# Optimization experiments

Hardware: AMD Instinct MI355X
Metric: run time of the kernel (lower is better)

## Reference

```python
import jax, jax.numpy as jnp
import numpy as np

B, N, M = 4, 2048, 2048
D_IN = 1024
H, HS = 16, 64
D_OUT = 1024


def _xavier(key, shape):
    # xavier_uniform over last two dims (fan_in=shape[-2], fan_out=shape[-1])
    fan_in, fan_out = shape[-2], shape[-1]
    limit = float(np.sqrt(6.0 / (fan_in + fan_out)))
    return jax.random.uniform(key, shape, jnp.float32, -limit, limit)


def setup_inputs() -> dict:
    key = jax.random.key(0)
    ks = jax.random.split(key, 7)
    return {
        "query": jax.random.normal(ks[0], (B, N, D_IN), jnp.float32),
        "key": jax.random.normal(ks[1], (B, M, D_IN), jnp.float32),
        "value": jax.random.normal(ks[2], (B, M, D_IN), jnp.float32),
        "query_kernel": _xavier(ks[3], (H, D_IN, HS)),
        "key_kernel": _xavier(ks[4], (H, D_IN, HS)),
        "value_kernel": _xavier(ks[5], (H, D_IN, HS)),
        "projection_kernel": _xavier(ks[6], (H, HS, D_OUT)),
        "projection_bias": jnp.zeros((D_OUT,), jnp.float32),
    }


def reference(query, key, value, query_kernel, key_kernel, value_kernel,
              projection_kernel, projection_bias):
    # per-head projections: (B, N, H, HS)
    q = jnp.einsum('bni,hio->bnho', query, query_kernel)
    k = jnp.einsum('bmi,hio->bmho', key, key_kernel)
    v = jnp.einsum('bmi,hio->bmho', value, value_kernel)
    q = q / jnp.sqrt(jnp.asarray(HS, q.dtype))
    logits = jnp.einsum('bnho,bmho->bhnm', q, k)          # (B, H, N, M)
    attn = jax.nn.softmax(logits, axis=-1)
    mh = jnp.einsum('bhnm,bmhi->bnhi', attn, v)           # (B, N, H, HS)
    out = jnp.einsum('bnhi,hio->bno', mh, projection_kernel) + projection_bias
    return out
```

## Files before the change

kernel.cpp:

```cpp
#include <hip/hip_runtime.h>

typedef __attribute__((ext_vector_type(8))) __bf16 bf16x8;
typedef __attribute__((ext_vector_type(4))) float f32x4;
typedef __attribute__((ext_vector_type(16))) float f32x16;
typedef __attribute__((ext_vector_type(8))) unsigned short u16x8;

__device__ __forceinline__ unsigned short f2bf(float f) {
  unsigned int u = __builtin_bit_cast(unsigned int, f);
  u += 0x7FFFu + ((u >> 16) & 1u);
  return (unsigned short)(u >> 16);
}
__device__ __forceinline__ unsigned int cvtpk(float a, float b) {
  unsigned int r;
  asm("v_cvt_pk_bf16_f32 %0, %1, %2" : "=v"(r) : "v"(a), "v"(b));
  return r;
}

#define KDIM 1024

__global__ __launch_bounds__(256) void prep_all(const float* __restrict__ wq,
                                                const float* __restrict__ wk,
                                                const float* __restrict__ wv,
                                                const float* __restrict__ wp,
                                                unsigned short* __restrict__ Wq,
                                                unsigned short* __restrict__ Wk,
                                                unsigned short* __restrict__ Wv,
                                                unsigned short* __restrict__ Wp,
                                                const float* __restrict__ q,
                                                const float* __restrict__ k,
                                                const float* __restrict__ v,
                                                unsigned short* __restrict__ qb,
                                                unsigned short* __restrict__ kb,
                                                unsigned short* __restrict__ vb) {
  __shared__ float T[64][68];
  const int t = threadIdx.x;
  if (blockIdx.x >= 1024) {
    const int blk = blockIdx.x - 1024;
    const int s3 = blk >> 12;
    const int inner = blk & 4095;
    const float* in = s3 == 0 ? q : (s3 == 1 ? k : v);
    unsigned short* out = s3 == 0 ? qb : (s3 == 1 ? kb : vb);
    const long i = ((long)inner * 256 + t) * 8;
    float4 a = *reinterpret_cast<const float4*>(in + i);
    float4 b = *reinterpret_cast<const float4*>(in + i + 4);
    uint4 o;
    o.x = cvtpk(a.x, a.y);
    o.y = cvtpk(a.z, a.w);
    o.z = cvtpk(b.x, b.y);
    o.w = cvtpk(b.z, b.w);
    *reinterpret_cast<uint4*>(out + i) = o;
    return;
  }
  const int sel = blockIdx.x >> 8;
  const int blk = blockIdx.x & 255;
  const int r = t >> 2, c0 = (t & 3) * 16;
  if (sel < 3) {
    const float* w = sel == 0 ? wq : (sel == 1 ? wk : wv);
    unsigned short* out = sel == 0 ? Wq : (sel == 1 ? Wk : Wv);
    const float scale = sel == 0 ? 0.125f * 1.44269504089f : 1.0f;
    const int h = blk >> 4;
    const int k0 = (blk & 15) * 64;
    const float* src = w + h * 65536 + (k0 + r) * 64 + c0;
#pragma unroll
    for (int e = 0; e < 16; e += 4)
      *reinterpret_cast<float4*>(&T[r][c0 + e]) = *reinterpret_cast<const float4*>(src + e);
    __syncthreads();
    unsigned int pk[8];
#pragma unroll
    for (int e = 0; e < 8; ++e)
      pk[e] = cvtpk(T[c0 + 2 * e][r] * scale, T[c0 + 2 * e + 1][r] * scale);
    unsigned short* dst = out + (h * 64 + r) * 1024 + k0 + c0;
    *reinterpret_cast<uint4*>(dst) = *reinterpret_cast<uint4*>(pk);
    *reinterpret_cast<uint4*>(dst + 8) = *reinterpret_cast<uint4*>(pk + 4);
  } else {
    const int i0 = (blk >> 4) * 64;
    const int o0 = (blk & 15) * 64;
    const float* src = wp + (long)(i0 + r) * 1024 + o0 + c0;
#pragma unroll
    for (int e = 0; e < 16; e += 4)
      *reinterpret_cast<float4*>(&T[r][c0 + e]) = *reinterpret_cast<const float4*>(src + e);
    __syncthreads();
    unsigned int pk[8];
#pragma unroll
    for (int e = 0; e < 8; ++e)
      pk[e] = cvtpk(T[c0 + 2 * e][r], T[c0 + 2 * e + 1][r]);
    unsigned short* dst = Wp + (long)(o0 + r) * 1024 + i0 + c0;
    *reinterpret_cast<uint4*>(dst) = *reinterpret_cast<uint4*>(pk);
    *reinterpret_cast<uint4*>(dst + 8) = *reinterpret_cast<uint4*>(pk + 4);
  }
}

#define STAGE_B(buf, kk)                                                                   \
  _Pragma("unroll") for (int i = 0; i < 4; ++i) {                                          \
    const int seg = w * 4 + i;                                                             \
    const int row = seg * 8 + rowl;                                                        \
    const unsigned short* src =                                                            \
        Wt + (long)(bx * 128 + row) * KDIM + (kk) + ((chnk ^ (row & 7)) * 8);              \
    __builtin_amdgcn_global_load_lds((const __attribute__((address_space(1))) void*)src,   \
                                     (__attribute__((address_space(3))) void*)&Bs[(buf) * 8192 + seg * 512], \
                                     16, 0, 0);                                            \
  }
#define STAGE_A(buf, kk)                                                                   \
  _Pragma("unroll") for (int i = 0; i < 4; ++i) {                                          \
    const int seg = w * 4 + i;                                                             \
    const int row = seg * 8 + rowl;                                                        \
    const unsigned short* src =                                                            \
        Ap + ((long)by * 128 + row) * KDIM + (kk) + ((chnk ^ (row & 7)) * 8);              \
    __builtin_amdgcn_global_load_lds((const __attribute__((address_space(1))) void*)src,   \
                                     (__attribute__((address_space(3))) void*)&As[(buf) * 8192 + seg * 512], \
                                     16, 0, 0);                                            \
  }
#define GEMM_COMPUTE(buf)                                                                  \
  _Pragma("unroll") for (int kc = 0; kc < 2; ++kc) {                                       \
    const int chs = ((kc * 4 + lh) ^ (l15 & 7)) * 8;                                       \
    bf16x8 af[4], bfr[4];                                                                  \
    _Pragma("unroll") for (int mi = 0; mi < 4; ++mi)                                       \
        af[mi] = *reinterpret_cast<const bf16x8*>(&As[(buf) * 8192 + (wr + mi * 16 + l15) * 64 + chs]); \
    _Pragma("unroll") for (int ni = 0; ni < 4; ++ni)                                       \
        bfr[ni] = *reinterpret_cast<const bf16x8*>(&Bs[(buf) * 8192 + (wc + ni * 16 + l15) * 64 + chs]); \
    _Pragma("unroll") for (int mi = 0; mi < 4; ++mi)                                       \
      _Pragma("unroll") for (int ni = 0; ni < 4; ++ni)                                     \
          acc[mi][ni] = __builtin_amdgcn_mfma_f32_16x16x32_bf16(af[mi], bfr[ni], acc[mi][ni], 0, 0, 0); \
  }

__global__ __launch_bounds__(256) void gemm_qkv(const unsigned short* __restrict__ qa,
                                                const unsigned short* __restrict__ ka,
                                                const unsigned short* __restrict__ va,
                                                const unsigned short* __restrict__ Wq,
                                                const unsigned short* __restrict__ Wk,
                                                const unsigned short* __restrict__ Wv,
                                                unsigned short* __restrict__ qo,
                                                unsigned short* __restrict__ ko,
                                                unsigned short* __restrict__ vo) {
  __shared__ unsigned short As[2 * 128 * 64];
  __shared__ unsigned short Bs[2 * 128 * 64];
  const int f = blockIdx.x;
  const int xcd = f & 7;
  const int bx = (f >> 3) & 7;
  const int by8 = (f >> 6) & 7;
  const int z = f >> 9;
  const int by = by8 * 8 + xcd;
  const unsigned short* Ap = z == 0 ? qa : (z == 1 ? ka : va);
  const unsigned short* Wt = z == 0 ? Wq : (z == 1 ? Wk : Wv);
  unsigned short* Cp = z == 0 ? qo : (z == 1 ? ko : vo);
  const int t = threadIdx.x;
  const int lane = t & 63, w = t >> 6;
  const int wr = (w >> 1) * 64, wc = (w & 1) * 64;
  const int l15 = lane & 15, lh = lane >> 4;
  const int rowl = lane >> 3;
  const int chnk = lane & 7;

  f32x4 acc[4][4];
#pragma unroll
  for (int i = 0; i < 4; ++i)
#pragma unroll
    for (int j = 0; j < 4; ++j) acc[i][j] = {0.f, 0.f, 0.f, 0.f};

  STAGE_B(0, 0)
  STAGE_A(0, 0)
  __syncthreads();
  for (int k0 = 0; k0 < KDIM; k0 += 64) {
    const int cur = (k0 >> 6) & 1;
    if (k0 + 64 < KDIM) {
      STAGE_B(cur ^ 1, k0 + 64)
      STAGE_A(cur ^ 1, k0 + 64)
    }
    GEMM_COMPUTE(cur)
    __syncthreads();
  }

  const long rbase = (long)by * 128 + wr;
  const long cbase = (long)bx * 128 + wc;
#pragma unroll
  for (int ni = 0; ni < 4; ++ni) {
    const long col = cbase + ni * 16 + l15;
#pragma unroll
    for (int mi = 0; mi < 4; ++mi) {
      const long row = rbase + mi * 16 + lh * 4;
      if (z == 2) {
        uint2 val;
        val.x = cvtpk(acc[mi][ni][0], acc[mi][ni][1]);
        val.y = cvtpk(acc[mi][ni][2], acc[mi][ni][3]);
        *reinterpret_cast<uint2*>(
            &Cp[(row >> 11) * 2097152 + col * 2048 + (row & 2047)]) = val;
      } else {
#pragma unroll
        for (int j = 0; j < 4; ++j)
          Cp[(row + j) * KDIM + col] = f2bf(acc[mi][ni][j]);
      }
    }
  }
}

__global__ __launch_bounds__(256) void gemm_out(const unsigned short* __restrict__ Ap,
                                                const unsigned short* __restrict__ Wt,
                                                float* __restrict__ Cp,
                                                const float* __restrict__ bias) {
  __shared__ unsigned short As[2 * 128 * 64];
  __shared__ unsigned short Bs[2 * 128 * 64];
  const int f = blockIdx.x;
  const int xcd = f & 7;
  const int bx = (f >> 3) & 7;
  const int by = ((f >> 6) & 7) * 8 + xcd;
  const int t = threadIdx.x;
  const int lane = t & 63, w = t >> 6;
  const int wr = (w >> 1) * 64, wc = (w & 1) * 64;
  const int l15 = lane & 15, lh = lane >> 4;
  const int rowl = lane >> 3;
  const int chnk = lane & 7;

  f32x4 acc[4][4];
#pragma unroll
  for (int i = 0; i < 4; ++i)
#pragma unroll
    for (int j = 0; j < 4; ++j) acc[i][j] = {0.f, 0.f, 0.f, 0.f};

  STAGE_B(0, 0)
  STAGE_A(0, 0)
  __syncthreads();
  for (int k0 = 0; k0 < KDIM; k0 += 64) {
    const int cur = (k0 >> 6) & 1;
    if (k0 + 64 < KDIM) {
      STAGE_B(cur ^ 1, k0 + 64)
      STAGE_A(cur ^ 1, k0 + 64)
    }
    GEMM_COMPUTE(cur)
    __syncthreads();
  }

  const long rbase = (long)by * 128 + wr;
  const long cbase = (long)bx * 128 + wc;
#pragma unroll
  for (int ni = 0; ni < 4; ++ni) {
    const long col = cbase + ni * 16 + l15;
    const float bv = bias[col];
#pragma unroll
    for (int mi = 0; mi < 4; ++mi) {
      const long row = rbase + mi * 16 + lh * 4;
#pragma unroll
      for (int j = 0; j < 4; ++j)
        Cp[(row + j) * KDIM + col] = acc[mi][ni][j] + bv;
    }
  }
}

__global__ __launch_bounds__(256, 2) void attn_k(const unsigned short* __restrict__ Qp,
                                                 const unsigned short* __restrict__ Kp,
                                                 const unsigned short* __restrict__ Vtg,
                                                 unsigned short* __restrict__ Op) {
  constexpr int LST = 72;
  __shared__ unsigned short Kl[64 * LST];
  __shared__ unsigned short Vl[64 * LST];
  const int t = threadIdx.x;
  const int lane = t & 63, w = t >> 6;
  const int l31 = lane & 31;
  const int hi = lane >> 5;
  const int d = blockIdx.x;
  const int xcd = d & 7, ii = d >> 3;
  const int bh = xcd * 8 + (ii >> 3);
  const int qblk = ii & 7;
  const long base = (long)(bh >> 4) * 2097152 + (long)(bh & 15) * 64;
  const long vbase = (long)bh * 131072;
  const int n0 = qblk * 256;
  const int sr = t >> 2, sc = (t & 3) * 16;

  bf16x8 qbA[4], qbB[4];
  {
    const unsigned short* qA = Qp + base + (long)(n0 + w * 64 + l31) * 1024 + hi * 8;
    const unsigned short* qB = qA + 32 * 1024;
#pragma unroll
    for (int kc = 0; kc < 4; ++kc) {
      qbA[kc] = *reinterpret_cast<const bf16x8*>(qA + kc * 16);
      qbB[kc] = *reinterpret_cast<const bf16x8*>(qB + kc * 16);
    }
  }

  const unsigned short* ksrc = Kp + base + (long)sr * 1024 + sc;
  const unsigned short* vsrc = Vtg + vbase + (long)sr * 2048 + sc;
  u16x8 kr0 = *reinterpret_cast<const u16x8*>(ksrc);
  u16x8 kr1 = *reinterpret_cast<const u16x8*>(ksrc + 8);
  u16x8 vr0 = *reinterpret_cast<const u16x8*>(vsrc);
  u16x8 vr1 = *reinterpret_cast<const u16x8*>(vsrc + 8);

  float lsumA = 0.f, lsumB = 0.f;
  f32x16 accA0, accA1, accB0, accB1;
#pragma unroll
  for (int r = 0; r < 16; ++r) { accA0[r] = 0.f; accA1[r] = 0.f; accB0[r] = 0.f; accB1[r] = 0.f; }

  for (int m0 = 0; m0 < 2048; m0 += 64) {
    *reinterpret_cast<u16x8*>(&Kl[sr * LST + sc]) = kr0;
    *reinterpret_cast<u16x8*>(&Kl[sr * LST + sc + 8]) = kr1;
    *reinterpret_cast<u16x8*>(&Vl[sr * LST + sc]) = vr0;
    *reinterpret_cast<u16x8*>(&Vl[sr * LST + sc + 8]) = vr1;
    __syncthreads();
    if (m0 + 64 < 2048) {
      kr0 = *reinterpret_cast<const u16x8*>(ksrc + (long)(m0 + 64) * 1024);
      kr1 = *reinterpret_cast<const u16x8*>(ksrc + (long)(m0 + 64) * 1024 + 8);
      vr0 = *reinterpret_cast<const u16x8*>(vsrc + m0 + 64);
      vr1 = *reinterpret_cast<const u16x8*>(vsrc + m0 + 72);
    }

    f32x16 sA0, sA1, sB0, sB1;
#pragma unroll
    for (int r = 0; r < 16; ++r) { sA0[r] = 0.f; sA1[r] = 0.f; sB0[r] = 0.f; sB1[r] = 0.f; }
    __builtin_amdgcn_s_setprio(1);
#pragma unroll
    for (int kc = 0; kc < 4; ++kc) {
      bf16x8 ka0 = *reinterpret_cast<const bf16x8*>(&Kl[(l31) * LST + kc * 16 + hi * 8]);
      bf16x8 ka1 = *reinterpret_cast<const bf16x8*>(&Kl[(32 + l31) * LST + kc * 16 + hi * 8]);
      sA0 = __builtin_amdgcn_mfma_f32_32x32x16_bf16(ka0, qbA[kc], sA0, 0, 0, 0);
      sA1 = __builtin_amdgcn_mfma_f32_32x32x16_bf16(ka1, qbA[kc], sA1, 0, 0, 0);
      sB0 = __builtin_amdgcn_mfma_f32_32x32x16_bf16(ka0, qbB[kc], sB0, 0, 0, 0);
      sB1 = __builtin_amdgcn_mfma_f32_32x32x16_bf16(ka1, qbB[kc], sB1, 0, 0, 0);
    }
    __builtin_amdgcn_s_setprio(0);

    float lstA = 0.f, lstB = 0.f;
#pragma unroll
    for (int r = 0; r < 16; ++r) {
      sA0[r] = __builtin_amdgcn_exp2f(sA0[r]);
      sA1[r] = __builtin_amdgcn_exp2f(sA1[r]);
      lstA += sA0[r] + sA1[r];
      sB0[r] = __builtin_amdgcn_exp2f(sB0[r]);
      sB1[r] = __builtin_amdgcn_exp2f(sB1[r]);
      lstB += sB0[r] + sB1[r];
    }
    lsumA += lstA;
    lsumB += lstB;

    unsigned int WA0[8], WA1[8], WB0[8], WB1[8];
#pragma unroll
    for (int j = 0; j < 8; ++j) {
      WA0[j] = cvtpk(sA0[2 * j], sA0[2 * j + 1]);
      WA1[j] = cvtpk(sA1[2 * j], sA1[2 * j + 1]);
      WB0[j] = cvtpk(sB0[2 * j], sB0[2 * j + 1]);
      WB1[j] = cvtpk(sB1[2 * j], sB1[2 * j + 1]);
    }

    __builtin_amdgcn_s_setprio(1);
#pragma unroll
    for (int kc4 = 0; kc4 < 4; ++kc4) {
      const unsigned int* WmA = (kc4 < 2) ? WA0 : WA1;
      const unsigned int* WmB = (kc4 < 2) ? WB0 : WB1;
      const int b = 4 * (kc4 & 1);
      unsigned int a1 = (unsigned int)__shfl_xor((int)(hi ? WmA[b] : WmA[b + 2]), 32);
      unsigned int a2 = (unsigned int)__shfl_xor((int)(hi ? WmA[b + 1] : WmA[b + 3]), 32);
      unsigned int b1 = (unsigned int)__shfl_xor((int)(hi ? WmB[b] : WmB[b + 2]), 32);
      unsigned int b2 = (unsigned int)__shfl_xor((int)(hi ? WmB[b + 1] : WmB[b + 3]), 32);
      union { unsigned int u[4]; bf16x8 v; } cA, cB;
      cA.u[0] = hi ? a1 : WmA[b];
      cA.u[1] = hi ? a2 : WmA[b + 1];
      cA.u[2] = hi ? WmA[b + 2] : a1;
      cA.u[3] = hi ? WmA[b + 3] : a2;
      cB.u[0] = hi ? b1 : WmB[b];
      cB.u[1] = hi ? b2 : WmB[b + 1];
      cB.u[2] = hi ? WmB[b + 2] : b1;
      cB.u[3] = hi ? WmB[b + 3] : b2;
      bf16x8 vb0 = *reinterpret_cast<const bf16x8*>(&Vl[(l31) * LST + kc4 * 16 + hi * 8]);
      bf16x8 vb1 = *reinterpret_cast<const bf16x8*>(&Vl[(32 + l31) * LST + kc4 * 16 + hi * 8]);
      accA0 = __builtin_amdgcn_mfma_f32_32x32x16_bf16(cA.v, vb0, accA0, 0, 0, 0);
      accA1 = __builtin_amdgcn_mfma_f32_32x32x16_bf16(cA.v, vb1, accA1, 0, 0, 0);
      accB0 = __builtin_amdgcn_mfma_f32_32x32x16_bf16(cB.v, vb0, accB0, 0, 0, 0);
      accB1 = __builtin_amdgcn_mfma_f32_32x32x16_bf16(cB.v, vb1, accB1, 0, 0, 0);
    }
    __builtin_amdgcn_s_setprio(0);
    __syncthreads();
  }

  lsumA += __shfl_xor(lsumA, 32);
  lsumB += __shfl_xor(lsumB, 32);
  float linvA = 1.f / lsumA;
  float linvB = 1.f / lsumB;
#pragma unroll
  for (int r = 0; r < 16; ++r) {
    const int qrow = (r & 3) + 8 * (r >> 2) + 4 * hi;
    float lrA = __shfl(linvA, qrow);
    float lrB = __shfl(linvB, qrow);
    const long rowA = n0 + w * 64 + qrow;
    const long rowB = rowA + 32;
    Op[base + rowA * 1024 + l31] = f2bf(accA0[r] * lrA);
    Op[base + rowA * 1024 + 32 + l31] = f2bf(accA1[r] * lrA);
    Op[base + rowB * 1024 + l31] = f2bf(accB0[r] * lrB);
    Op[base + rowB * 1024 + 32 + l31] = f2bf(accB1[r] * lrB);
  }
}

extern "C" void kernel_launch(void* const* d_in, const int* in_sizes, int n_in,
                              void* d_out, int out_size, void* d_ws, size_t ws_size,
                              hipStream_t stream) {
  const float* q    = (const float*)d_in[0];
  const float* k    = (const float*)d_in[1];
  const float* v    = (const float*)d_in[2];
  const float* wq   = (const float*)d_in[3];
  const float* wk   = (const float*)d_in[4];
  const float* wv   = (const float*)d_in[5];
  const float* wp   = (const float*)d_in[6];
  const float* bias = (const float*)d_in[7];

  unsigned short* ws = (unsigned short*)d_ws;
  unsigned short* Wq = ws;
  unsigned short* Wk = Wq + (1 << 20);
  unsigned short* Wv = Wk + (1 << 20);
  unsigned short* Wp = Wv + (1 << 20);
  unsigned short* qp = Wp + (1 << 20);
  unsigned short* kp = qp + (8 << 20);
  unsigned short* vt = kp + (8 << 20);
  unsigned short* mh = vt + (8 << 20);

  unsigned short* qb16 = (unsigned short*)d_out;
  unsigned short* kb16 = qb16 + (8 << 20);
  unsigned short* vb16 = mh;

  prep_all<<<13312, 256, 0, stream>>>(wq, wk, wv, wp, Wq, Wk, Wv, Wp,
                                      q, k, v, qb16, kb16, vb16);

  gemm_qkv<<<1536, 256, 0, stream>>>(qb16, kb16, vb16, Wq, Wk, Wv, qp, kp, vt);

  attn_k<<<512, 256, 0, stream>>>(qp, kp, vt, mh);

  gemm_out<<<512, 256, 0, stream>>>(mh, Wp, (float*)d_out, bias);
}
```

Before: 183.1 us.

## Double-buffer K/V tiles in LDS to drop one barrier per iteration

Splits the K and V shared-memory tiles into two buffers. The next tile's registers are stored into the alternate buffer after the QK MFMAs, and the following tile's global loads are issued after the PV MFMAs. This removes one __syncthreads per iteration and overlaps the LDS writes with the softmax work. In exchange it doubles LDS use, and the global prefetch now has less compute to hide behind before it is consumed.

Measured after the change: 183.6 us. No clear change (+0.3%).

```diff
diff --git a/kernel.cpp b/kernel.cpp
--- a/kernel.cpp
+++ b/kernel.cpp
@@ -249,8 +249,8 @@
                                                  const unsigned short* __restrict__ Vtg,
                                                  unsigned short* __restrict__ Op) {
   constexpr int LST = 72;
-  __shared__ unsigned short Kl[64 * LST];
-  __shared__ unsigned short Vl[64 * LST];
+  __shared__ unsigned short Kl[2][64 * LST];
+  __shared__ unsigned short Vl[2][64 * LST];
   const int t = threadIdx.x;
   const int lane = t & 63, w = t >> 6;
   const int l31 = lane & 31;
@@ -277,28 +277,30 @@
 
   const unsigned short* ksrc = Kp + base + (long)sr * 1024 + sc;
   const unsigned short* vsrc = Vtg + vbase + (long)sr * 2048 + sc;
+
   u16x8 kr0 = *reinterpret_cast<const u16x8*>(ksrc);
   u16x8 kr1 = *reinterpret_cast<const u16x8*>(ksrc + 8);
   u16x8 vr0 = *reinterpret_cast<const u16x8*>(vsrc);
   u16x8 vr1 = *reinterpret_cast<const u16x8*>(vsrc + 8);
+  *reinterpret_cast<u16x8*>(&Kl[0][sr * LST + sc]) = kr0;
+  *reinterpret_cast<u16x8*>(&Kl[0][sr * LST + sc + 8]) = kr1;
+  *reinterpret_cast<u16x8*>(&Vl[0][sr * LST + sc]) = vr0;
+  *reinterpret_cast<u16x8*>(&Vl[0][sr * LST + sc + 8]) = vr1;
+  kr0 = *reinterpret_cast<const u16x8*>(ksrc + 64 * 1024);
+  kr1 = *reinterpret_cast<const u16x8*>(ksrc + 64 * 1024 + 8);
+  vr0 = *reinterpret_cast<const u16x8*>(vsrc + 64);
+  vr1 = *reinterpret_cast<const u16x8*>(vsrc + 72);
+  __syncthreads();
 
   float lsumA = 0.f, lsumB = 0.f;
   f32x16 accA0, accA1, accB0, accB1;
 #pragma unroll
   for (int r = 0; r < 16; ++r) { accA0[r] = 0.f; accA1[r] = 0.f; accB0[r] = 0.f; accB1[r] = 0.f; }
 
-  for (int m0 = 0; m0 < 2048; m0 += 64) {
-    *reinterpret_cast<u16x8*>(&Kl[sr * LST + sc]) = kr0;
-    *reinterpret_cast<u16x8*>(&Kl[sr * LST + sc + 8]) = kr1;
-    *reinterpret_cast<u16x8*>(&Vl[sr * LST + sc]) = vr0;
-    *reinterpret_cast<u16x8*>(&Vl[sr * LST + sc + 8]) = vr1;
-    __syncthreads();
-    if (m0 + 64 < 2048) {
-      kr0 = *reinterpret_cast<const u16x8*>(ksrc + (long)(m0 + 64) * 1024);
-      kr1 = *reinterpret_cast<const u16x8*>(ksrc + (long)(m0 + 64) * 1024 + 8);
-      vr0 = *reinterpret_cast<const u16x8*>(vsrc + m0 + 64);
-      vr1 = *reinterpret_cast<const u16x8*>(vsrc + m0 + 72);
-    }
+  for (int tI = 0; tI < 32; ++tI) {
+    const int cur = tI & 1;
+    const unsigned short* Kc = &Kl[cur][0];
+    const unsigned short* Vc = &Vl[cur][0];
 
     f32x16 sA0, sA1, sB0, sB1;
 #pragma unroll
@@ -306,14 +308,23 @@
     __builtin_amdgcn_s_setprio(1);
 #pragma unroll
     for (int kc = 0; kc < 4; ++kc) {
-      bf16x8 ka0 = *reinterpret_cast<const bf16x8*>(&Kl[(l31) * LST + kc * 16 + hi * 8]);
-      bf16x8 ka1 = *reinterpret_cast<const bf16x8*>(&Kl[(32 + l31) * LST + kc * 16 + hi * 8]);
+      bf16x8 ka0 = *reinterpret_cast<const bf16x8*>(&Kc[(l31) * LST + kc * 16 + hi * 8]);
+      bf16x8 ka1 = *reinterpret_cast<const bf16x8*>(&Kc[(32 + l31) * LST + kc * 16 + hi * 8]);
       sA0 = __builtin_amdgcn_mfma_f32_32x32x16_bf16(ka0, qbA[kc], sA0, 0, 0, 0);
       sA1 = __builtin_amdgcn_mfma_f32_32x32x16_bf16(ka1, qbA[kc], sA1, 0, 0, 0);
       sB0 = __builtin_amdgcn_mfma_f32_32x32x16_bf16(ka0, qbB[kc], sB0, 0, 0, 0);
       sB1 = __builtin_amdgcn_mfma_f32_32x32x16_bf16(ka1, qbB[kc], sB1, 0, 0, 0);
     }
     __builtin_amdgcn_s_setprio(0);
+
+    if (tI < 31) {
+      unsigned short* Kn = &Kl[cur ^ 1][0];
+      unsigned short* Vn = &Vl[cur ^ 1][0];
+      *reinterpret_cast<u16x8*>(&Kn[sr * LST + sc]) = kr0;
+      *reinterpret_cast<u16x8*>(&Kn[sr * LST + sc + 8]) = kr1;
+      *reinterpret_cast<u16x8*>(&Vn[sr * LST + sc]) = vr0;
+      *reinterpret_cast<u16x8*>(&Vn[sr * LST + sc + 8]) = vr1;
+    }
 
     float lstA = 0.f, lstB = 0.f;
 #pragma unroll
@@ -356,14 +367,22 @@
       cB.u[1] = hi ? b2 : WmB[b + 1];
       cB.u[2] = hi ? WmB[b + 2] : b1;
       cB.u[3] = hi ? WmB[b + 3] : b2;
-      bf16x8 vb0 = *reinterpret_cast<const bf16x8*>(&Vl[(l31) * LST + kc4 * 16 + hi * 8]);
-      bf16x8 vb1 = *reinterpret_cast<const bf16x8*>(&Vl[(32 + l31) * LST + kc4 * 16 + hi * 8]);
+      bf16x8 vb0 = *reinterpret_cast<const bf16x8*>(&Vc[(l31) * LST + kc4 * 16 + hi * 8]);
+      bf16x8 vb1 = *reinterpret_cast<const bf16x8*>(&Vc[(32 + l31) * LST + kc4 * 16 + hi * 8]);
       accA0 = __builtin_amdgcn_mfma_f32_32x32x16_bf16(cA.v, vb0, accA0, 0, 0, 0);
       accA1 = __builtin_amdgcn_mfma_f32_32x32x16_bf16(cA.v, vb1, accA1, 0, 0, 0);
       accB0 = __builtin_amdgcn_mfma_f32_32x32x16_bf16(cB.v, vb0, accB0, 0, 0, 0);
       accB1 = __builtin_amdgcn_mfma_f32_32x32x16_bf16(cB.v, vb1, accB1, 0, 0, 0);
     }
     __builtin_amdgcn_s_setprio(0);
+
+    if (tI < 30) {
+      const long off = (long)(tI + 2) * 64;
+      kr0 = *reinterpret_cast<const u16x8*>(ksrc + off * 1024);
+      kr1 = *reinterpret_cast<const u16x8*>(ksrc + off * 1024 + 8);
+      vr0 = *reinterpret_cast<const u16x8*>(vsrc + off);
+      vr1 = *reinterpret_cast<const u16x8*>(vsrc + off + 8);
+    }
     __syncthreads();
   }
 
```

## Software-pipeline attention loop: overlap QK of tile t with PV of tile t-1

Applied to the files above, without the earlier changes.

Restructures the attention inner loop into a software pipeline. Each iteration computes QK^T MFMAs for the current tile while running the PV MFMAs for the previous tile's softmaxed probabilities, held in ping-pong P registers. K is double-buffered and V triple-buffered in LDS so there is one barrier per iteration. It also seeds the first QK MFMA with a zero constant instead of zero-initialising the accumulators. The aim is to hide exp/convert latency behind matrix work, at the cost of more registers and LDS, which may reduce occupancy.

Result: slower. 395.6 us (+116.0%).

```diff
diff --git a/kernel.cpp b/kernel.cpp
--- a/kernel.cpp
+++ b/kernel.cpp
@@ -249,8 +249,8 @@
                                                  const unsigned short* __restrict__ Vtg,
                                                  unsigned short* __restrict__ Op) {
   constexpr int LST = 72;
-  __shared__ unsigned short Kl[64 * LST];
-  __shared__ unsigned short Vl[64 * LST];
+  __shared__ unsigned short Kl[2][64 * LST];
+  __shared__ unsigned short Vl[3][64 * LST];
   const int t = threadIdx.x;
   const int lane = t & 63, w = t >> 6;
   const int l31 = lane & 31;
@@ -264,6 +264,10 @@
   const int n0 = qblk * 256;
   const int sr = t >> 2, sc = (t & 3) * 16;
 
+  f32x16 FZERO;
+#pragma unroll
+  for (int r = 0; r < 16; ++r) FZERO[r] = 0.f;
+
   bf16x8 qbA[4], qbB[4];
   {
     const unsigned short* qA = Qp + base + (long)(n0 + w * 64 + l31) * 1024 + hi * 8;
@@ -277,95 +281,144 @@
 
   const unsigned short* ksrc = Kp + base + (long)sr * 1024 + sc;
   const unsigned short* vsrc = Vtg + vbase + (long)sr * 2048 + sc;
+
+  float lsumA = 0.f, lsumB = 0.f;
+  f32x16 accA0 = FZERO, accA1 = FZERO, accB0 = FZERO, accB1 = FZERO;
+  unsigned int P0[32], P1[32];
+
+#define DO_QK(tI)                                                                          \
+  {                                                                                        \
+    const unsigned short* Kc = &Kl[(tI) & 1][0];                                           \
+    __builtin_amdgcn_s_setprio(1);                                                         \
+    {                                                                                      \
+      bf16x8 ka0 = *reinterpret_cast<const bf16x8*>(&Kc[(l31) * LST + hi * 8]);            \
+      bf16x8 ka1 = *reinterpret_cast<const bf16x8*>(&Kc[(32 + l31) * LST + hi * 8]);       \
+      sA0 = __builtin_amdgcn_mfma_f32_32x32x16_bf16(ka0, qbA[0], FZERO, 0, 0, 0);          \
+      sA1 = __builtin_amdgcn_mfma_f32_32x32x16_bf16(ka1, qbA[0], FZERO, 0, 0, 0);          \
+      sB0 = __builtin_amdgcn_mfma_f32_32x32x16_bf16(ka0, qbB[0], FZERO, 0, 0, 0);          \
+      sB1 = __builtin_amdgcn_mfma_f32_32x32x16_bf16(ka1, qbB[0], FZERO, 0, 0, 0);          \
+    }                                                                                      \
+    _Pragma("unroll") for (int kc = 1; kc < 4; ++kc) {                                     \
+      bf16x8 ka0 = *reinterpret_cast<const bf16x8*>(&Kc[(l31) * LST + kc * 16 + hi * 8]);  \
+      bf16x8 ka1 = *reinterpret_cast<const bf16x8*>(&Kc[(32 + l31) * LST + kc * 16 + hi * 8]); \
+      sA0 = __builtin_amdgcn_mfma_f32_32x32x16_bf16(ka0, qbA[kc], sA0, 0, 0, 0);           \
+      sA1 = __builtin_amdgcn_mfma_f32_32x32x16_bf16(ka1, qbA[kc], sA1, 0, 0, 0);           \
+      sB0 = __builtin_amdgcn_mfma_f32_32x32x16_bf16(ka0, qbB[kc], sB0, 0, 0, 0);           \
+      sB1 = __builtin_amdgcn_mfma_f32_32x32x16_bf16(ka1, qbB[kc], sB1, 0, 0, 0);           \
+    }                                                                                      \
+    __builtin_amdgcn_s_setprio(0);                                                         \
+  }
+
+#define DO_STAGE(kb, vb)                                                                   \
+  {                                                                                        \
+    *reinterpret_cast<u16x8*>(&Kl[kb][sr * LST + sc]) = kr0;                               \
+    *reinterpret_cast<u16x8*>(&Kl[kb][sr * LST + sc + 8]) = kr1;                           \
+    *reinterpret_cast<u16x8*>(&Vl[vb][sr * LST + sc]) = vr0;                               \
+    *reinterpret_cast<u16x8*>(&Vl[vb][sr * LST + sc + 8]) = vr1;                           \
+  }
+
+#define DO_PV(PR, vb)                                                                      \
+  {                                                                                        \
+    const unsigned short* Vc = &Vl[vb][0];                                                 \
+    __builtin_amdgcn_s_setprio(1);                                                         \
+    _Pragma("unroll") for (int kc4 = 0; kc4 < 4; ++kc4) {                                  \
+      const int offA = (kc4 < 2) ? 0 : 8;                                                  \
+      const int offB = offA + 16;                                                          \
+      const int b = 4 * (kc4 & 1);                                                         \
+      unsigned int a1 = (unsigned int)__shfl_xor((int)(hi ? PR[offA + b] : PR[offA + b + 2]), 32); \
+      unsigned int a2 = (unsigned int)__shfl_xor((int)(hi ? PR[offA + b + 1] : PR[offA + b + 3]), 32); \
+      unsigned int b1 = (unsigned int)__shfl_xor((int)(hi ? PR[offB + b] : PR[offB + b + 2]), 32); \
+      unsigned int b2 = (unsigned int)__shfl_xor((int)(hi ? PR[offB + b + 1] : PR[offB + b + 3]), 32); \
+      union { unsigned int u[4]; bf16x8 v; } cA, cB;                                       \
+      cA.u[0] = hi ? a1 : PR[offA + b];                                                    \
+      cA.u[1] = hi ? a2 : PR[offA + b + 1];                                                \
+      cA.u[2] = hi ? PR[offA + b + 2] : a1;                                                \
+      cA.u[3] = hi ? PR[offA + b + 3] : a2;                                                \
+      cB.u[0] = hi ? b1 : PR[offB + b];                                                    \
+      cB.u[1] = hi ? b2 : PR[offB + b + 1];                                                \
+      cB.u[2] = hi ? PR[offB + b + 2] : b1;                                                \
+      cB.u[3] = hi ? PR[offB + b + 3] : b2;                                                \
+      bf16x8 vb0 = *reinterpret_cast<const bf16x8*>(&Vc[(l31) * LST + kc4 * 16 + hi * 8]); \
+      bf16x8 vb1 = *reinterpret_cast<const bf16x8*>(&Vc[(32 + l31) * LST + kc4 * 16 + hi * 8]); \
+      accA0 = __builtin_amdgcn_mfma_f32_32x32x16_bf16(cA.v, vb0, accA0, 0, 0, 0);          \
+      accA1 = __builtin_amdgcn_mfma_f32_32x32x16_bf16(cA.v, vb1, accA1, 0, 0, 0);          \
+      accB0 = __builtin_amdgcn_mfma_f32_32x32x16_bf16(cB.v, vb0, accB0, 0, 0, 0);          \
+      accB1 = __builtin_amdgcn_mfma_f32_32x32x16_bf16(cB.v, vb1, accB1, 0, 0, 0);          \
+    }                                                                                      \
+    __builtin_amdgcn_s_setprio(0);                                                         \
+  }
+
+#define DO_SOFTMAX(PW)                                                                     \
+  {                                                                                        \
+    float lstA = 0.f, lstB = 0.f;                                                          \
+    _Pragma("unroll") for (int r = 0; r < 16; ++r) {                                       \
+      sA0[r] = __builtin_amdgcn_exp2f(sA0[r]);                                             \
+      sA1[r] = __builtin_amdgcn_exp2f(sA1[r]);                                             \
+      lstA += sA0[r] + sA1[r];                                                             \
+      sB0[r] = __builtin_amdgcn_exp2f(sB0[r]);                                             \
+      sB1[r] = __builtin_amdgcn_exp2f(sB1[r]);                                             \
+      lstB += sB0[r] + sB1[r];                                                             \
+    }                                                                                      \
+    lsumA += lstA;                                                                         \
+    lsumB += lstB;                                                                         \
+    _Pragma("unroll") for (int j = 0; j < 8; ++j) {                                        \
+      PW[j]      = cvtpk(sA0[2 * j], sA0[2 * j + 1]);                                      \
+      PW[8 + j]  = cvtpk(sA1[2 * j], sA1[2 * j + 1]);                                      \
+      PW[16 + j] = cvtpk(sB0[2 * j], sB0[2 * j + 1]);                                      \
+      PW[24 + j] = cvtpk(sB1[2 * j], sB1[2 * j + 1]);                                      \
+    }                                                                                      \
+  }
+
+#define DO_PREFETCH(nt)                                                                    \
+  {                                                                                        \
+    const long off = (long)(nt) * 64;                                                      \
+    kr0 = *reinterpret_cast<const u16x8*>(ksrc + off * 1024);                              \
+    kr1 = *reinterpret_cast<const u16x8*>(ksrc + off * 1024 + 8);                          \
+    vr0 = *reinterpret_cast<const u16x8*>(vsrc + off);                                     \
+    vr1 = *reinterpret_cast<const u16x8*>(vsrc + off + 8);                                 \
+  }
+
+#define BODY(tI, PW, PR)                                                                   \
+  {                                                                                        \
+    f32x16 sA0, sA1, sB0, sB1;                                                             \
+    DO_QK(tI)                                                                              \
+    if ((tI) < 31) DO_STAGE(((tI) + 1) & 1, ((tI) + 1) % 3)                                \
+    DO_PV(PR, ((tI) + 2) % 3)                                                              \
+    DO_SOFTMAX(PW)                                                                         \
+    if ((tI) < 30) DO_PREFETCH((tI) + 2)                                                   \
+    __syncthreads();                                                                       \
+  }
+
   u16x8 kr0 = *reinterpret_cast<const u16x8*>(ksrc);
   u16x8 kr1 = *reinterpret_cast<const u16x8*>(ksrc + 8);
   u16x8 vr0 = *reinterpret_cast<const u16x8*>(vsrc);
   u16x8 vr1 = *reinterpret_cast<const u16x8*>(vsrc + 8);
-
-  float lsumA = 0.f, lsumB = 0.f;
-  f32x16 accA0, accA1, accB0, accB1;
-#pragma unroll
-  for (int r = 0; r < 16; ++r) { accA0[r] = 0.f; accA1[r] = 0.f; accB0[r] = 0.f; accB1[r] = 0.f; }
-
-  for (int m0 = 0; m0 < 2048; m0 += 64) {
-    *reinterpret_cast<u16x8*>(&Kl[sr * LST + sc]) = kr0;
-    *reinterpret_cast<u16x8*>(&Kl[sr * LST + sc + 8]) = kr1;
-    *reinterpret_cast<u16x8*>(&Vl[sr * LST + sc]) = vr0;
-    *reinterpret_cast<u16x8*>(&Vl[sr * LST + sc + 8]) = vr1;
+  DO_STAGE(0, 0)
+  DO_PREFETCH(1)
+  __syncthreads();
+  {
+    f32x16 sA0, sA1, sB0, sB1;
+    DO_QK(0)
+    DO_STAGE(1, 1)
+    DO_SOFTMAX(P0)
+    DO_PREFETCH(2)
     __syncthreads();
-    if (m0 + 64 < 2048) {
-      kr0 = *reinterpret_cast<const u16x8*>(ksrc + (long)(m0 + 64) * 1024);
-      kr1 = *reinterpret_cast<const u16x8*>(ksrc + (long)(m0 + 64) * 1024 + 8);
-      vr0 = *reinterpret_cast<const u16x8*>(vsrc + m0 + 64);
-      vr1 = *reinterpret_cast<const u16x8*>(vsrc + m0 + 72);
-    }
-
-    f32x16 sA0, sA1, sB0, sB1;
-#pragma unroll
-    for (int r = 0; r < 16; ++r) { sA0[r] = 0.f; sA1[r] = 0.f; sB0[r] = 0.f; sB1[r] = 0.f; }
-    __builtin_amdgcn_s_setprio(1);
-#pragma unroll
-    for (int kc = 0; kc < 4; ++kc) {
-      bf16x8 ka0 = *reinterpret_cast<const bf16x8*>(&Kl[(l31) * LST + kc * 16 + hi * 8]);
-      bf16x8 ka1 = *reinterpret_cast<const bf16x8*>(&Kl[(32 + l31) * LST + kc * 16 + hi * 8]);
-      sA0 = __builtin_amdgcn_mfma_f32_32x32x16_bf16(ka0, qbA[kc], sA0, 0, 0, 0);
-      sA1 = __builtin_amdgcn_mfma_f32_32x32x16_bf16(ka1, qbA[kc], sA1, 0, 0, 0);
-      sB0 = __builtin_amdgcn_mfma_f32_32x32x16_bf16(ka0, qbB[kc], sB0, 0, 0, 0);
-      sB1 = __builtin_amdgcn_mfma_f32_32x32x16_bf16(ka1, qbB[kc], sB1, 0, 0, 0);
-    }
-    __builtin_amdgcn_s_setprio(0);
-
-    float lstA = 0.f, lstB = 0.f;
-#pragma unroll
-    for (int r = 0; r < 16; ++r) {
-      sA0[r] = __builtin_amdgcn_exp2f(sA0[r]);
-      sA1[r] = __builtin_amdgcn_exp2f(sA1[r]);
-      lstA += sA0[r] + sA1[r];
-      sB0[r] = __builtin_amdgcn_exp2f(sB0[r]);
-      sB1[r] = __builtin_amdgcn_exp2f(sB1[r]);
-      lstB += sB0[r] + sB1[r];
-    }
-    lsumA += lstA;
-    lsumB += lstB;
-
-    unsigned int WA0[8], WA1[8], WB0[8], WB1[8];
-#pragma unroll
-    for (int j = 0; j < 8; ++j) {
-      WA0[j] = cvtpk(sA0[2 * j], sA0[2 * j + 1]);
-      WA1[j] = cvtpk(sA1[2 * j], sA1[2 * j + 1]);
-      WB0[j] = cvtpk(sB0[2 * j], sB0[2 * j + 1]);
-      WB1[j] = cvtpk(sB1[2 * j], sB1[2 * j + 1]);
-    }
-
-    __builtin_amdgcn_s_setprio(1);
-#pragma unroll
-    for (int kc4 = 0; kc4 < 4; ++kc4) {
-      const unsigned int* WmA = (kc4 < 2) ? WA0 : WA1;
-      const unsigned int* WmB = (kc4 < 2) ? WB0 : WB1;
-      const int b = 4 * (kc4 & 1);
-      unsigned int a1 = (unsigned int)__shfl_xor((int)(hi ? WmA[b] : WmA[b + 2]), 32);
-      unsigned int a2 = (unsigned int)__shfl_xor((int)(hi ? WmA[b + 1] : WmA[b + 3]), 32);
-      unsigned int b1 = (unsigned int)__shfl_xor((int)(hi ? WmB[b] : WmB[b + 2]), 32);
-      unsigned int b2 = (unsigned int)__shfl_xor((int)(hi ? WmB[b + 1] : WmB[b + 3]), 32);
-      union { unsigned int u[4]; bf16x8 v; } cA, cB;
-      cA.u[0] = hi ? a1 : WmA[b];
-      cA.u[1] = hi ? a2 : WmA[b + 1];
-      cA.u[2] = hi ? WmA[b + 2] : a1;
-      cA.u[3] = hi ? WmA[b + 3] : a2;
-      cB.u[0] = hi ? b1 : WmB[b];
-      cB.u[1] = hi ? b2 : WmB[b + 1];
-      cB.u[2] = hi ? WmB[b + 2] : b1;
-      cB.u[3] = hi ? WmB[b + 3] : b2;
-      bf16x8 vb0 = *reinterpret_cast<const bf16x8*>(&Vl[(l31) * LST + kc4 * 16 + hi * 8]);
-      bf16x8 vb1 = *reinterpret_cast<const bf16x8*>(&Vl[(32 + l31) * LST + kc4 * 16 + hi * 8]);
-      accA0 = __builtin_amdgcn_mfma_f32_32x32x16_bf16(cA.v, vb0, accA0, 0, 0, 0);
-      accA1 = __builtin_amdgcn_mfma_f32_32x32x16_bf16(cA.v, vb1, accA1, 0, 0, 0);
-      accB0 = __builtin_amdgcn_mfma_f32_32x32x16_bf16(cB.v, vb0, accB0, 0, 0, 0);
-      accB1 = __builtin_amdgcn_mfma_f32_32x32x16_bf16(cB.v, vb1, accB1, 0, 0, 0);
-    }
-    __builtin_amdgcn_s_setprio(0);
-    __syncthreads();
-  }
+  }
+
+  for (int tp = 0; tp < 15; ++tp) {
+    const int t1 = 2 * tp + 1;
+    BODY(t1, P1, P0)
+    BODY(t1 + 1, P0, P1)
+  }
+  BODY(31, P1, P0)
+  DO_PV(P1, 1)
+
+#undef BODY
+#undef DO_PREFETCH
+#undef DO_SOFTMAX
+#undef DO_PV
+#undef DO_STAGE
+#undef DO_QK
 
   lsumA += __shfl_xor(lsumA, 32);
   lsumB += __shfl_xor(lsumB, 32);
```
